# Kernel optimization log

Hardware: AMD Instinct MI355X
Metric: run time of the kernel (lower is better)

## Reference

```python
import jax, jax.numpy as jnp
import numpy as np

EMBED_DIM = 512
KDIM = 64
VDIM = 64


def setup_inputs() -> dict:
    key = jax.random.key(0)
    kx, kq, kk, kv = jax.random.split(key, 4)
    B, S = 4, 4096
    x = jax.random.normal(kx, (B, S, EMBED_DIM), dtype=jnp.float32)
    # nn.Linear(embed_dim, out) weight has shape [out, embed_dim]
    WQ = jax.random.normal(kq, (KDIM, EMBED_DIM), dtype=jnp.float32) * (EMBED_DIM ** -0.5)
    WK = jax.random.normal(kk, (KDIM, EMBED_DIM), dtype=jnp.float32) * (EMBED_DIM ** -0.5)
    WV = jax.random.normal(kv, (VDIM, EMBED_DIM), dtype=jnp.float32) * (EMBED_DIM ** -0.5)
    return {"x": x, "WQ": WQ, "WK": WK, "WV": WV}


def reference(x, WQ, WK, WV):
    # q,k: [B,S,kdim]; v: [B,S,vdim] (self-attention: x[0] is x[-1])
    q = jnp.einsum('bse,ke->bsk', x, WQ)
    k = jnp.einsum('bse,ke->bsk', x, WK)
    v = jnp.einsum('bse,ve->bsv', x, WV)
    scale = k.shape[-1] ** -0.5
    scores = jnp.einsum('bqk,bsk->bqs', q, k) * scale  # [B,S,S]
    # dropout p=0.0 -> identity; masked branch in source is a no-op (non-in-place masked_fill discarded)
    attn = jax.nn.softmax(scores, axis=-1)
    out = jnp.einsum('bqs,bsv->bqv', attn, v)  # [B,S,vdim]
    return out
```

## Files before the change

### kernel.cpp

```cpp
#include <hip/hip_runtime.h>

#define BATCH 4
#define SEQ   4096
#define EMB   512
#define HD    64

typedef __attribute__((ext_vector_type(8))) short short8;
typedef __attribute__((ext_vector_type(4))) float floatx4;

static __device__ __forceinline__ unsigned short f2bf(float f) {
  unsigned u = __builtin_bit_cast(unsigned, f);
  u += 0x7fffu + ((u >> 16) & 1u);
  return (unsigned short)(u >> 16);
}
static __device__ __forceinline__ float bf2f(unsigned short h) {
  unsigned u = ((unsigned)h) << 16;
  return __builtin_bit_cast(float, u);
}
static __device__ __forceinline__ unsigned pack_hi16(float lo, float hi) {
#if __has_builtin(__builtin_amdgcn_perm)
  return __builtin_amdgcn_perm(__builtin_bit_cast(unsigned, hi),
                               __builtin_bit_cast(unsigned, lo), 0x07060302u);
#else
  return (__builtin_bit_cast(unsigned, lo) >> 16) |
         (__builtin_bit_cast(unsigned, hi) & 0xffff0000u);
#endif
}

__global__ __launch_bounds__(256) void convw_kernel(
    const float* __restrict__ WQ, const float* __restrict__ WK,
    const float* __restrict__ WV, unsigned short* __restrict__ Wpk)
{
  int t = blockIdx.x * 256 + threadIdx.x;
  int p    = t >> 12;
  int w    = (t >> 10) & 3;
  int kc   = (t >> 6) & 15;
  int lane = t & 63;
  int lr = lane & 15, g = lane >> 4;
  const float* src = (p == 0) ? WQ : ((p == 1) ? WK : WV);
  const float4* s4 = (const float4*)(src + (16 * w + lr) * EMB + kc * 32 + 8 * g);
  float4 a = s4[0], b = s4[1];
  float vv[8] = {a.x, a.y, a.z, a.w, b.x, b.y, b.z, b.w};
  short8 o;
#pragma unroll
  for (int j = 0; j < 8; ++j) {
    unsigned short h = f2bf(vv[j]);
    o[j] = (p == 3) ? (short)f2bf(vv[j] - bf2f(h)) : (short)h;
  }
  *(short8*)(Wpk + (size_t)t * 8) = o;
}

#define XST 40

__global__ __launch_bounds__(256) void proj_kernel(
    const float* __restrict__ x,
    const unsigned short* __restrict__ Wpk,
    unsigned short* __restrict__ Qb,
    unsigned short* __restrict__ Kb,
    unsigned short* __restrict__ VTb)
{
  __shared__ __align__(16) unsigned short Xh[2][32 * XST];
  __shared__ __align__(16) unsigned short Xl[2][32 * XST];

  const int tid  = threadIdx.x;
  const int lane = tid & 63;
  const int w    = tid >> 6;
  const int lr   = lane & 15, g = lane >> 4;
  const long rowBase = (long)blockIdx.x * 32;

  floatx4 accQ[2], accK[2], accV[2];
#pragma unroll
  for (int rt = 0; rt < 2; ++rt) {
    floatx4 z = {0.f, 0.f, 0.f, 0.f};
    accQ[rt] = z; accK[rt] = z; accV[rt] = z;
  }

  const int srow = tid >> 3;
  const int sc   = 4 * (tid & 7);

  auto stagex = [&](int kc, int buf) {
    float4 v = *(const float4*)(x + (rowBase + srow) * EMB + kc * 32 + sc);
    float vv[4] = {v.x, v.y, v.z, v.w};
    ushort4 hi, lo;
#pragma unroll
    for (int i = 0; i < 4; ++i) {
      unsigned short h = f2bf(vv[i]);
      ((unsigned short*)&hi)[i] = h;
      ((unsigned short*)&lo)[i] = f2bf(vv[i] - bf2f(h));
    }
    *(ushort4*)&Xh[buf][srow * XST + sc] = hi;
    *(ushort4*)&Xl[buf][srow * XST + sc] = lo;
  };

  stagex(0, 0);
#pragma unroll 2
  for (int kc = 0; kc < 16; ++kc) {
    __syncthreads();
    if (kc + 1 < 16) stagex(kc + 1, (kc + 1) & 1);
    const int buf = kc & 1;
    const unsigned short* wb = Wpk + (size_t)(w * 16 + kc) * 512 + lane * 8;
    short8 wq  = *(const short8*)(wb);
    short8 wk  = *(const short8*)(wb + 32768);
    short8 wvh = *(const short8*)(wb + 2 * 32768);
    short8 wvl = *(const short8*)(wb + 3 * 32768);
#pragma unroll
    for (int rt = 0; rt < 2; ++rt) {
      short8 xh = *(const short8*)&Xh[buf][(16 * rt + lr) * XST + 8 * g];
      short8 xl = *(const short8*)&Xl[buf][(16 * rt + lr) * XST + 8 * g];
      accQ[rt] = __builtin_amdgcn_mfma_f32_16x16x32_bf16(wq, xh, accQ[rt], 0, 0, 0);
      accK[rt] = __builtin_amdgcn_mfma_f32_16x16x32_bf16(wk, xh, accK[rt], 0, 0, 0);
      accV[rt] = __builtin_amdgcn_mfma_f32_16x16x32_bf16(xh, wvh, accV[rt], 0, 0, 0);
      accV[rt] = __builtin_amdgcn_mfma_f32_16x16x32_bf16(xl, wvh, accV[rt], 0, 0, 0);
      accV[rt] = __builtin_amdgcn_mfma_f32_16x16x32_bf16(xh, wvl, accV[rt], 0, 0, 0);
    }
  }

  const int bb  = (int)(rowBase >> 12);
  const int sIn = (int)(rowBase & 4095);
#pragma unroll
  for (int rt = 0; rt < 2; ++rt) {
    {
      long row = rowBase + 16 * rt + lr;
      int  col = 16 * w + 4 * g;
      ushort4 u; u.x = f2bf(accQ[rt][0]); u.y = f2bf(accQ[rt][1]);
      u.z = f2bf(accQ[rt][2]); u.w = f2bf(accQ[rt][3]);
      *(ushort4*)(Qb + row * HD + col) = u;
      ushort4 v; v.x = f2bf(accK[rt][0]); v.y = f2bf(accK[rt][1]);
      v.z = f2bf(accK[rt][2]); v.w = f2bf(accK[rt][3]);
      *(ushort4*)(Kb + row * HD + col) = v;
    }
    {
      long addr = ((long)(bb * 64 + 16 * w + lr)) * SEQ + sIn + 16 * rt + 4 * g;
      ushort4 u; u.x = f2bf(accV[rt][0]); u.y = f2bf(accV[rt][1]);
      u.z = f2bf(accV[rt][2]); u.w = f2bf(accV[rt][3]);
      *(ushort4*)(VTb + addr) = u;
    }
  }
}

#define PST 72

__global__ __launch_bounds__(256) void flash_kernel(
    const unsigned short* __restrict__ Qb,
    const unsigned short* __restrict__ Kb,
    const unsigned short* __restrict__ VTb,
    float* __restrict__ Opart, float* __restrict__ Lpart)
{
  __shared__ __align__(16) unsigned short K0lds[64 * 64];
  __shared__ __align__(16) unsigned short V0lds[64 * 64];
  __shared__ __align__(16) unsigned short K1lds[64 * 64];
  __shared__ __align__(16) unsigned short V1lds[64 * 64];
  __shared__ __align__(16) unsigned short Plds[4][32 * PST];

  const int tid  = threadIdx.x;
  const int lane = tid & 63;
  const int w    = tid >> 6;
  const int lr   = lane & 15, g = lane >> 4;
  const int qb   = blockIdx.x >> 2;
  const int ks   = blockIdx.x & 3;
  const int b    = qb >> 5;
  const int qt   = qb & 31;
  const long qrow0 = (long)b * SEQ + qt * 128 + 32 * w;
  const int  kbase = ks * 1024;

  short8 qf[2][2];
#pragma unroll
  for (int qh = 0; qh < 2; ++qh)
#pragma unroll
    for (int ec = 0; ec < 2; ++ec)
      qf[qh][ec] = *(const short8*)(Qb + (qrow0 + 16 * qh + lr) * HD + ec * 32 + 8 * g);

  floatx4 accO[2][4];
#pragma unroll
  for (int qh = 0; qh < 2; ++qh)
#pragma unroll
    for (int t = 0; t < 4; ++t) { floatx4 z = {0.f,0.f,0.f,0.f}; accO[qh][t] = z; }
  float lsum[2] = {0.0f, 0.0f};
  const float cp = 0.18033688011112042f;
  const float SH = 2.0f;

#define STAGE(kt_, KL, VL) do {                                               \
    const int k0_ = kbase + (kt_) * 64;                                       \
    _Pragma("unroll")                                                         \
    for (int h_ = 0; h_ < 2; ++h_) {                                          \
      int ci_  = h_ * 256 + tid;                                              \
      int row_ = ci_ >> 3;                                                    \
      int cc_  = (ci_ & 7) ^ (row_ & 7);                                      \
      const unsigned short* gK_ = Kb + ((long)b * SEQ + k0_ + row_) * HD + cc_ * 8; \
      __builtin_amdgcn_global_load_lds(                                       \
          (const __attribute__((address_space(1))) void*)gK_,                 \
          (__attribute__((address_space(3))) void*)((KL) + ci_ * 8), 16, 0, 0); \
      const unsigned short* gV_ = VTb + ((long)b * HD + row_) * SEQ + k0_ + cc_ * 8; \
      __builtin_amdgcn_global_load_lds(                                       \
          (const __attribute__((address_space(1))) void*)gV_,                 \
          (__attribute__((address_space(3))) void*)((VL) + ci_ * 8), 16, 0, 0); \
    }                                                                         \
  } while (0)

#define COMPUTE(KL, VL) do {                                                  \
    floatx4 s_[2][4];                                                         \
    _Pragma("unroll")                                                         \
    for (int qh = 0; qh < 2; ++qh)                                            \
      _Pragma("unroll")                                                       \
      for (int t = 0; t < 4; ++t) { floatx4 z = {0.f,0.f,0.f,0.f}; s_[qh][t] = z; } \
    _Pragma("unroll")                                                         \
    for (int ec = 0; ec < 2; ++ec) {                                          \
      _Pragma("unroll")                                                       \
      for (int t = 0; t < 4; ++t) {                                           \
        int key  = 16 * t + lr;                                               \
        int slot = key * 8 + ((4 * ec + g) ^ (key & 7));                      \
        short8 kf = *(const short8*)((KL) + slot * 8);                        \
        s_[0][t] = __builtin_amdgcn_mfma_f32_16x16x32_bf16(kf, qf[0][ec], s_[0][t], 0, 0, 0); \
        s_[1][t] = __builtin_amdgcn_mfma_f32_16x16x32_bf16(kf, qf[1][ec], s_[1][t], 0, 0, 0); \
      }                                                                       \
    }                                                                         \
    _Pragma("unroll")                                                         \
    for (int qh = 0; qh < 2; ++qh) {                                          \
      unsigned short* prow = &Plds[w][(16 * qh + lr) * PST];                  \
      float ls = 0.0f;                                                        \
      _Pragma("unroll")                                                       \
      for (int t = 0; t < 4; ++t) {                                           \
        float p0 = __builtin_amdgcn_exp2f(__builtin_fmaf(s_[qh][t][0], cp, -SH)); \
        float p1 = __builtin_amdgcn_exp2f(__builtin_fmaf(s_[qh][t][1], cp, -SH)); \
        float p2 = __builtin_amdgcn_exp2f(__builtin_fmaf(s_[qh][t][2], cp, -SH)); \
        float p3 = __builtin_amdgcn_exp2f(__builtin_fmaf(s_[qh][t][3], cp, -SH)); \
        uint2 u;                                                              \
        u.x = pack_hi16(p0, p1);                                              \
        u.y = pack_hi16(p2, p3);                                              \
        ls += __builtin_bit_cast(float, u.x << 16);                           \
        ls += __builtin_bit_cast(float, u.x & 0xffff0000u);                   \
        ls += __builtin_bit_cast(float, u.y << 16);                           \
        ls += __builtin_bit_cast(float, u.y & 0xffff0000u);                   \
        *(uint2*)(prow + 16 * t + 4 * g) = u;                                 \
      }                                                                       \
      lsum[qh] += ls;                                                         \
    }                                                                         \
    _Pragma("unroll")                                                         \
    for (int c = 0; c < 2; ++c) {                                             \
      short8 pf0 = *(const short8*)(&Plds[w][(     lr) * PST + 32 * c + 8 * g]); \
      short8 pf1 = *(const short8*)(&Plds[w][(16 + lr) * PST + 32 * c + 8 * g]); \
      _Pragma("unroll")                                                       \
      for (int t = 0; t < 4; ++t) {                                           \
        int d    = 16 * t + lr;                                               \
        int slot = d * 8 + ((4 * c + g) ^ (d & 7));                           \
        short8 vf = *(const short8*)((VL) + slot * 8);                        \
        accO[0][t] = __builtin_amdgcn_mfma_f32_16x16x32_bf16(vf, pf0, accO[0][t], 0, 0, 0); \
        accO[1][t] = __builtin_amdgcn_mfma_f32_16x16x32_bf16(vf, pf1, accO[1][t], 0, 0, 0); \
      }                                                                       \
    }                                                                         \
  } while (0)

  STAGE(0, K0lds, V0lds);
  for (int kt = 0; kt < 16; kt += 2) {
    __syncthreads();
    STAGE(kt + 1, K1lds, V1lds);
    COMPUTE(K0lds, V0lds);
    __syncthreads();
    if (kt + 2 < 16) STAGE(kt + 2, K0lds, V0lds);
    COMPUTE(K1lds, V1lds);
  }
#undef STAGE
#undef COMPUTE

  float* obase = Opart + (size_t)(qb * 4 + ks) * 128 * HD;
#pragma unroll
  for (int qh = 0; qh < 2; ++qh) {
    float l = lsum[qh];
    l += __shfl_xor(l, 16, 64);
    l += __shfl_xor(l, 32, 64);
    int qlocal = 32 * w + 16 * qh + lr;
#pragma unroll
    for (int t = 0; t < 4; ++t) {
      float4 o = {accO[qh][t][0], accO[qh][t][1], accO[qh][t][2], accO[qh][t][3]};
      *(float4*)(obase + qlocal * HD + 16 * t + 4 * g) = o;
    }
    if (g == 0) Lpart[(qb * 4 + ks) * 128 + qlocal] = l;
  }
}

__global__ __launch_bounds__(256) void combine_kernel(
    const float* __restrict__ Opart, const float* __restrict__ Lpart,
    float* __restrict__ out)
{
  int t   = blockIdx.x * 256 + threadIdx.x;
  int row = t >> 4;
  int d0  = (t & 15) * 4;
  int qb = row >> 7, qi = row & 127;
  float4 acc = {0.f, 0.f, 0.f, 0.f};
  float lt = 0.0f;
#pragma unroll
  for (int ks = 0; ks < 4; ++ks) {
    const float* p = Opart + ((size_t)(qb * 4 + ks) * 128 + qi) * HD + d0;
    float4 v = *(const float4*)p;
    acc.x += v.x; acc.y += v.y; acc.z += v.z; acc.w += v.w;
    lt += Lpart[(qb * 4 + ks) * 128 + qi];
  }
  float inv = 1.0f / lt;
  float4 o = {acc.x * inv, acc.y * inv, acc.z * inv, acc.w * inv};
  *(float4*)(out + (size_t)row * HD + d0) = o;
}

extern "C" void kernel_launch(void* const* d_in, const int* in_sizes, int n_in,
                              void* d_out, int out_size, void* d_ws, size_t ws_size,
                              hipStream_t stream) {
  const float* x  = (const float*)d_in[0];
  const float* WQ = (const float*)d_in[1];
  const float* WK = (const float*)d_in[2];
  const float* WV = (const float*)d_in[3];

  unsigned short* Qb  = (unsigned short*)d_ws;
  unsigned short* Kb  = Qb  + (size_t)BATCH * SEQ * HD;
  unsigned short* VTb = Kb  + (size_t)BATCH * SEQ * HD;
  unsigned short* Wpk = VTb + (size_t)BATCH * SEQ * HD;
  float* Opart = (float*)(Wpk + 262144);
  float* Lpart = Opart + (size_t)128 * 4 * 128 * HD;

  convw_kernel<<<64, 256, 0, stream>>>(WQ, WK, WV, Wpk);
  proj_kernel<<<(BATCH * SEQ) / 32, 256, 0, stream>>>(x, Wpk, Qb, Kb, VTb);
  flash_kernel<<<512, 256, 0, stream>>>(Qb, Kb, VTb, Opart, Lpart);
  combine_kernel<<<1024, 256, 0, stream>>>(Opart, Lpart, (float*)d_out);
}
```

Before: 122.3 us.

## Enlarge flash query tile to 256 rows, split keys eight ways, store fp16 partials

The flash kernel now has each wave handle 64 query rows instead of 32, so every K/V fragment loaded from LDS feeds twice as many MFMAs. Keys are split into 8 chunks of 512 rather than 4 of 1024, which keeps the grid at 512 blocks. Partial outputs are written as fp16 instead of fp32, halving the partial-output traffic into the combine kernel at some precision cost. The projection kernel also issues the global x load two iterations ahead to hide its latency, and the larger register and LDS footprint (launch_bounds 256,2) may reduce occupancy.

```diff
diff --git a/kernel.cpp b/kernel.cpp
--- a/kernel.cpp
+++ b/kernel.cpp
@@ -25,6 +25,21 @@
   return (__builtin_bit_cast(unsigned, lo) >> 16) |
          (__builtin_bit_cast(unsigned, hi) & 0xffff0000u);
 #endif
+}
+static __device__ __forceinline__ unsigned pack_f16(float a, float b) {
+#if __has_builtin(__builtin_amdgcn_cvt_pkrtz)
+  typedef __fp16 fp16v2 __attribute__((ext_vector_type(2)));
+  fp16v2 h = __builtin_amdgcn_cvt_pkrtz(a, b);
+  return __builtin_bit_cast(unsigned, h);
+#else
+  _Float16 ha = (_Float16)a, hb = (_Float16)b;
+  return (unsigned)__builtin_bit_cast(unsigned short, ha) |
+         ((unsigned)__builtin_bit_cast(unsigned short, hb) << 16);
+#endif
+}
+static __device__ __forceinline__ float f16_to_f32(unsigned short bits) {
+  _Float16 h = __builtin_bit_cast(_Float16, bits);
+  return (float)h;
 }
 
 __global__ __launch_bounds__(256) void convw_kernel(
@@ -77,9 +92,9 @@
 
   const int srow = tid >> 3;
   const int sc   = 4 * (tid & 7);
-
-  auto stagex = [&](int kc, int buf) {
-    float4 v = *(const float4*)(x + (rowBase + srow) * EMB + kc * 32 + sc);
+  const float* xbase = x + (rowBase + srow) * EMB + sc;
+
+  auto stage_write = [&](float4 v, int buf) {
     float vv[4] = {v.x, v.y, v.z, v.w};
     ushort4 hi, lo;
 #pragma unroll
@@ -92,17 +107,21 @@
     *(ushort4*)&Xl[buf][srow * XST + sc] = lo;
   };
 
-  stagex(0, 0);
+  float4 xv = *(const float4*)(xbase);
+  stage_write(xv, 0);
+  float4 xnxt = *(const float4*)(xbase + 32);
+
 #pragma unroll 2
   for (int kc = 0; kc < 16; ++kc) {
     __syncthreads();
-    if (kc + 1 < 16) stagex(kc + 1, (kc + 1) & 1);
-    const int buf = kc & 1;
     const unsigned short* wb = Wpk + (size_t)(w * 16 + kc) * 512 + lane * 8;
     short8 wq  = *(const short8*)(wb);
     short8 wk  = *(const short8*)(wb + 32768);
     short8 wvh = *(const short8*)(wb + 2 * 32768);
     short8 wvl = *(const short8*)(wb + 3 * 32768);
+    float4 xfut;
+    if (kc + 2 < 16) xfut = *(const float4*)(xbase + (kc + 2) * 32);
+    const int buf = kc & 1;
 #pragma unroll
     for (int rt = 0; rt < 2; ++rt) {
       short8 xh = *(const short8*)&Xh[buf][(16 * rt + lr) * XST + 8 * g];
@@ -113,6 +132,7 @@
       accV[rt] = __builtin_amdgcn_mfma_f32_16x16x32_bf16(xl, wvh, accV[rt], 0, 0, 0);
       accV[rt] = __builtin_amdgcn_mfma_f32_16x16x32_bf16(xh, wvl, accV[rt], 0, 0, 0);
     }
+    if (kc + 1 < 16) { stage_write(xnxt, (kc + 1) & 1); xnxt = xfut; }
   }
 
   const int bb  = (int)(rowBase >> 12);
@@ -140,42 +160,42 @@
 
 #define PST 72
 
-__global__ __launch_bounds__(256) void flash_kernel(
+__global__ __launch_bounds__(256, 2) void flash_kernel(
     const unsigned short* __restrict__ Qb,
     const unsigned short* __restrict__ Kb,
     const unsigned short* __restrict__ VTb,
-    float* __restrict__ Opart, float* __restrict__ Lpart)
+    unsigned short* __restrict__ Opart,
+    float* __restrict__ Lpart)
 {
   __shared__ __align__(16) unsigned short K0lds[64 * 64];
   __shared__ __align__(16) unsigned short V0lds[64 * 64];
   __shared__ __align__(16) unsigned short K1lds[64 * 64];
   __shared__ __align__(16) unsigned short V1lds[64 * 64];
-  __shared__ __align__(16) unsigned short Plds[4][32 * PST];
+  __shared__ __align__(16) unsigned short Plds[4][64 * PST];
 
   const int tid  = threadIdx.x;
   const int lane = tid & 63;
   const int w    = tid >> 6;
   const int lr   = lane & 15, g = lane >> 4;
-  const int qb   = blockIdx.x >> 2;
-  const int ks   = blockIdx.x & 3;
-  const int b    = qb >> 5;
-  const int qt   = qb & 31;
-  const long qrow0 = (long)b * SEQ + qt * 128 + 32 * w;
-  const int  kbase = ks * 1024;
-
-  short8 qf[2][2];
-#pragma unroll
-  for (int qh = 0; qh < 2; ++qh)
+  const int qb   = blockIdx.x >> 3;
+  const int ks   = blockIdx.x & 7;
+  const int bb   = qb >> 4;
+  const long qrow0 = (long)qb * 256 + 64 * w;
+  const int  kbase = ks * 512;
+
+  short8 qf[4][2];
+#pragma unroll
+  for (int qh = 0; qh < 4; ++qh)
 #pragma unroll
     for (int ec = 0; ec < 2; ++ec)
       qf[qh][ec] = *(const short8*)(Qb + (qrow0 + 16 * qh + lr) * HD + ec * 32 + 8 * g);
 
-  floatx4 accO[2][4];
-#pragma unroll
-  for (int qh = 0; qh < 2; ++qh)
+  floatx4 accO[4][4];
+#pragma unroll
+  for (int qh = 0; qh < 4; ++qh)
 #pragma unroll
     for (int t = 0; t < 4; ++t) { floatx4 z = {0.f,0.f,0.f,0.f}; accO[qh][t] = z; }
-  float lsum[2] = {0.0f, 0.0f};
+  float lsum[4] = {0.f, 0.f, 0.f, 0.f};
   const float cp = 0.18033688011112042f;
   const float SH = 2.0f;
 
@@ -186,11 +206,11 @@
       int ci_  = h_ * 256 + tid;                                              \
       int row_ = ci_ >> 3;                                                    \
       int cc_  = (ci_ & 7) ^ (row_ & 7);                                      \
-      const unsigned short* gK_ = Kb + ((long)b * SEQ + k0_ + row_) * HD + cc_ * 8; \
+      const unsigned short* gK_ = Kb + ((long)bb * SEQ + k0_ + row_) * HD + cc_ * 8; \
       __builtin_amdgcn_global_load_lds(                                       \
           (const __attribute__((address_space(1))) void*)gK_,                 \
           (__attribute__((address_space(3))) void*)((KL) + ci_ * 8), 16, 0, 0); \
-      const unsigned short* gV_ = VTb + ((long)b * HD + row_) * SEQ + k0_ + cc_ * 8; \
+      const unsigned short* gV_ = VTb + ((long)bb * HD + row_) * SEQ + k0_ + cc_ * 8; \
       __builtin_amdgcn_global_load_lds(                                       \
           (const __attribute__((address_space(1))) void*)gV_,                 \
           (__attribute__((address_space(3))) void*)((VL) + ci_ * 8), 16, 0, 0); \
@@ -198,32 +218,33 @@
   } while (0)
 
 #define COMPUTE(KL, VL) do {                                                  \
-    floatx4 s_[2][4];                                                         \
-    _Pragma("unroll")                                                         \
-    for (int qh = 0; qh < 2; ++qh)                                            \
-      _Pragma("unroll")                                                       \
-      for (int t = 0; t < 4; ++t) { floatx4 z = {0.f,0.f,0.f,0.f}; s_[qh][t] = z; } \
-    _Pragma("unroll")                                                         \
-    for (int ec = 0; ec < 2; ++ec) {                                          \
+    short8 kf[2][4];                                                          \
+    _Pragma("unroll")                                                         \
+    for (int ec = 0; ec < 2; ++ec)                                            \
       _Pragma("unroll")                                                       \
       for (int t = 0; t < 4; ++t) {                                           \
         int key  = 16 * t + lr;                                               \
         int slot = key * 8 + ((4 * ec + g) ^ (key & 7));                      \
-        short8 kf = *(const short8*)((KL) + slot * 8);                        \
-        s_[0][t] = __builtin_amdgcn_mfma_f32_16x16x32_bf16(kf, qf[0][ec], s_[0][t], 0, 0, 0); \
-        s_[1][t] = __builtin_amdgcn_mfma_f32_16x16x32_bf16(kf, qf[1][ec], s_[1][t], 0, 0, 0); \
+        kf[ec][t] = *(const short8*)((KL) + slot * 8);                        \
       }                                                                       \
-    }                                                                         \
-    _Pragma("unroll")                                                         \
-    for (int qh = 0; qh < 2; ++qh) {                                          \
+    _Pragma("unroll")                                                         \
+    for (int qh = 0; qh < 4; ++qh) {                                          \
+      floatx4 s_[4];                                                          \
+      _Pragma("unroll")                                                       \
+      for (int t = 0; t < 4; ++t) { floatx4 z = {0.f,0.f,0.f,0.f}; s_[t] = z; } \
+      _Pragma("unroll")                                                       \
+      for (int ec = 0; ec < 2; ++ec)                                          \
+        _Pragma("unroll")                                                     \
+        for (int t = 0; t < 4; ++t)                                           \
+          s_[t] = __builtin_amdgcn_mfma_f32_16x16x32_bf16(kf[ec][t], qf[qh][ec], s_[t], 0, 0, 0); \
       unsigned short* prow = &Plds[w][(16 * qh + lr) * PST];                  \
       float ls = 0.0f;                                                        \
       _Pragma("unroll")                                                       \
       for (int t = 0; t < 4; ++t) {                                           \
-        float p0 = __builtin_amdgcn_exp2f(__builtin_fmaf(s_[qh][t][0], cp, -SH)); \
-        float p1 = __builtin_amdgcn_exp2f(__builtin_fmaf(s_[qh][t][1], cp, -SH)); \
-        float p2 = __builtin_amdgcn_exp2f(__builtin_fmaf(s_[qh][t][2], cp, -SH)); \
-        float p3 = __builtin_amdgcn_exp2f(__builtin_fmaf(s_[qh][t][3], cp, -SH)); \
+        float p0 = __builtin_amdgcn_exp2f(__builtin_fmaf(s_[t][0], cp, -SH)); \
+        float p1 = __builtin_amdgcn_exp2f(__builtin_fmaf(s_[t][1], cp, -SH)); \
+        float p2 = __builtin_amdgcn_exp2f(__builtin_fmaf(s_[t][2], cp, -SH)); \
+        float p3 = __builtin_amdgcn_exp2f(__builtin_fmaf(s_[t][3], cp, -SH)); \
         uint2 u;                                                              \
         u.x = pack_hi16(p0, p1);                                              \
         u.y = pack_hi16(p2, p3);                                              \
@@ -235,65 +256,75 @@
       }                                                                       \
       lsum[qh] += ls;                                                         \
     }                                                                         \
-    _Pragma("unroll")                                                         \
-    for (int c = 0; c < 2; ++c) {                                             \
-      short8 pf0 = *(const short8*)(&Plds[w][(     lr) * PST + 32 * c + 8 * g]); \
-      short8 pf1 = *(const short8*)(&Plds[w][(16 + lr) * PST + 32 * c + 8 * g]); \
+    short8 vf[2][4];                                                          \
+    _Pragma("unroll")                                                         \
+    for (int c = 0; c < 2; ++c)                                               \
       _Pragma("unroll")                                                       \
       for (int t = 0; t < 4; ++t) {                                           \
         int d    = 16 * t + lr;                                               \
         int slot = d * 8 + ((4 * c + g) ^ (d & 7));                           \
-        short8 vf = *(const short8*)((VL) + slot * 8);                        \
-        accO[0][t] = __builtin_amdgcn_mfma_f32_16x16x32_bf16(vf, pf0, accO[0][t], 0, 0, 0); \
-        accO[1][t] = __builtin_amdgcn_mfma_f32_16x16x32_bf16(vf, pf1, accO[1][t], 0, 0, 0); \
+        vf[c][t] = *(const short8*)((VL) + slot * 8);                         \
       }                                                                       \
-    }                                                                         \
+    _Pragma("unroll")                                                         \
+    for (int qh = 0; qh < 4; ++qh)                                            \
+      _Pragma("unroll")                                                       \
+      for (int c = 0; c < 2; ++c) {                                           \
+        short8 pf = *(const short8*)(&Plds[w][(16 * qh + lr) * PST + 32 * c + 8 * g]); \
+        _Pragma("unroll")                                                     \
+        for (int t = 0; t < 4; ++t)                                           \
+          accO[qh][t] = __builtin_amdgcn_mfma_f32_16x16x32_bf16(vf[c][t], pf, accO[qh][t], 0, 0, 0); \
+      }                                                                       \
   } while (0)
 
   STAGE(0, K0lds, V0lds);
-  for (int kt = 0; kt < 16; kt += 2) {
+  for (int kt = 0; kt < 8; kt += 2) {
     __syncthreads();
     STAGE(kt + 1, K1lds, V1lds);
     COMPUTE(K0lds, V0lds);
     __syncthreads();
-    if (kt + 2 < 16) STAGE(kt + 2, K0lds, V0lds);
+    if (kt + 2 < 8) STAGE(kt + 2, K0lds, V0lds);
     COMPUTE(K1lds, V1lds);
   }
 #undef STAGE
 #undef COMPUTE
 
-  float* obase = Opart + (size_t)(qb * 4 + ks) * 128 * HD;
-#pragma unroll
-  for (int qh = 0; qh < 2; ++qh) {
+  unsigned short* obase = Opart + (size_t)(qb * 8 + ks) * 256 * HD;
+#pragma unroll
+  for (int qh = 0; qh < 4; ++qh) {
     float l = lsum[qh];
     l += __shfl_xor(l, 16, 64);
     l += __shfl_xor(l, 32, 64);
-    int qlocal = 32 * w + 16 * qh + lr;
+    int qlocal = 64 * w + 16 * qh + lr;
 #pragma unroll
     for (int t = 0; t < 4; ++t) {
-      float4 o = {accO[qh][t][0], accO[qh][t][1], accO[qh][t][2], accO[qh][t][3]};
-      *(float4*)(obase + qlocal * HD + 16 * t + 4 * g) = o;
-    }
-    if (g == 0) Lpart[(qb * 4 + ks) * 128 + qlocal] = l;
+      uint2 u;
+      u.x = pack_f16(accO[qh][t][0], accO[qh][t][1]);
+      u.y = pack_f16(accO[qh][t][2], accO[qh][t][3]);
+      *(uint2*)(obase + qlocal * HD + 16 * t + 4 * g) = u;
+    }
+    if (g == 0) Lpart[(qb * 8 + ks) * 256 + qlocal] = l;
   }
 }
 
 __global__ __launch_bounds__(256) void combine_kernel(
-    const float* __restrict__ Opart, const float* __restrict__ Lpart,
+    const unsigned short* __restrict__ Opart, const float* __restrict__ Lpart,
     float* __restrict__ out)
 {
   int t   = blockIdx.x * 256 + threadIdx.x;
   int row = t >> 4;
   int d0  = (t & 15) * 4;
-  int qb = row >> 7, qi = row & 127;
+  int qb = row >> 8, qi = row & 255;
   float4 acc = {0.f, 0.f, 0.f, 0.f};
   float lt = 0.0f;
 #pragma unroll
-  for (int ks = 0; ks < 4; ++ks) {
-    const float* p = Opart + ((size_t)(qb * 4 + ks) * 128 + qi) * HD + d0;
-    float4 v = *(const float4*)p;
-    acc.x += v.x; acc.y += v.y; acc.z += v.z; acc.w += v.w;
-    lt += Lpart[(qb * 4 + ks) * 128 + qi];
+  for (int ks = 0; ks < 8; ++ks) {
+    const unsigned short* p = Opart + ((size_t)(qb * 8 + ks) * 256 + qi) * HD + d0;
+    ushort4 v = *(const ushort4*)p;
+    acc.x += f16_to_f32(v.x);
+    acc.y += f16_to_f32(v.y);
+    acc.z += f16_to_f32(v.z);
+    acc.w += f16_to_f32(v.w);
+    lt += Lpart[(qb * 8 + ks) * 256 + qi];
   }
   float inv = 1.0f / lt;
   float4 o = {acc.x * inv, acc.y * inv, acc.z * inv, acc.w * inv};
@@ -312,8 +343,8 @@
   unsigned short* Kb  = Qb  + (size_t)BATCH * SEQ * HD;
   unsigned short* VTb = Kb  + (size_t)BATCH * SEQ * HD;
   unsigned short* Wpk = VTb + (size_t)BATCH * SEQ * HD;
-  float* Opart = (float*)(Wpk + 262144);
-  float* Lpart = Opart + (size_t)128 * 4 * 128 * HD;
+  unsigned short* Opart = Wpk + 262144;
+  float* Lpart = (float*)(Opart + (size_t)512 * 256 * HD);
 
   convw_kernel<<<64, 256, 0, stream>>>(WQ, WK, WV, Wpk);
   proj_kernel<<<(BATCH * SEQ) / 32, 256, 0, stream>>>(x, Wpk, Qb, Kb, VTb);
```

Measured after the change: 119.5 us (median of 2 runs). -2.3%, faster.
